# Kernel tuning notes

Hardware: AMD Instinct MI355X
Metric: run time of the kernel (lower is better)

Reference implementation:

```python
import jax, jax.numpy as jnp
import numpy as np

NOPE = 128          # qk_nope_head_dim
ROPE = 64           # qk_rope_head_dim
KV_LORA = 512       # kv_lora_rank
SCALE = (KV_LORA + ROPE) ** (-0.5)


def setup_inputs() -> dict:
    key = jax.random.key(0)
    k1, k2, k3, k4, k5 = jax.random.split(key, 5)
    T, H, K, S = 512, 128, 512, 8192
    q = jax.random.normal(k1, (T, H, NOPE + ROPE), dtype=jnp.float32)
    kv_cache = jax.random.normal(k2, (S, KV_LORA + ROPE), dtype=jnp.float32)
    topk_indices = jax.random.randint(k3, (T, K), 0, S, dtype=jnp.int32)
    k_b_proj_trans = jax.random.normal(k4, (H, KV_LORA, NOPE), dtype=jnp.float32) * 0.02
    v_b_proj = jax.random.normal(k5, (H, 128, KV_LORA), dtype=jnp.float32) * 0.02
    return {"q": q, "kv_cache": kv_cache, "topk_indices": topk_indices,
            "k_b_proj_trans": k_b_proj_trans, "v_b_proj": v_b_proj}


def reference(q, kv_cache, topk_indices, k_b_proj_trans, v_b_proj):
    # q: [T, H, 192]; kv_cache: [S, 576]; topk_indices: [T, K]
    q_nope, q_rope = q[..., :NOPE], q[..., NOPE:]
    # bmm_out(q_nope_t, k_b_proj_trans.transpose(1,2)): [T,H,128] x [H,512,128] -> [T,H,512]
    q_lat = jnp.einsum('thd,hkd->thk', q_nope, k_b_proj_trans)
    q_concat = jnp.concatenate([q_lat, q_rope], axis=-1)        # [T, H, 576]
    # sparse MLA: gather selected latent KV per token
    kv_sel = kv_cache[topk_indices]                              # [T, K, 576]
    scores = jnp.einsum('thc,tkc->thk', q_concat, kv_sel) * SCALE
    p = jax.nn.softmax(scores, axis=-1)                          # [T, H, K]
    attn_lat = jnp.einsum('thk,tkc->thc', p, kv_sel[..., :KV_LORA])  # [T, H, 512]
    # bmm_out(attn_lat_t, v_b_proj.transpose(1,2)): [T,H,512] x [H,512,128] -> [T,H,128]
    out = jnp.einsum('thc,hvc->thv', attn_lat, v_b_proj)
    return out
```

## Files before the change

kernel.cpp:

```cpp
#include <hip/hip_runtime.h>
#include <stdint.h>


#define SCALE 0.041666666666666664f

typedef __bf16 bf16x8 __attribute__((ext_vector_type(8)));
typedef float floatx4 __attribute__((ext_vector_type(4)));
typedef unsigned int uint32x2 __attribute__((ext_vector_type(2)));
typedef unsigned int uint32x4 __attribute__((ext_vector_type(4)));

static __device__ __forceinline__ unsigned short f2bf(float f) {
  unsigned int u = __builtin_bit_cast(unsigned int, f);
  u += 0x7FFF + ((u >> 16) & 1);
  return (unsigned short)(u >> 16);
}
static __device__ __forceinline__ float bf2f(unsigned short h) {
  unsigned int u = ((unsigned int)h) << 16;
  return __builtin_bit_cast(float, u);
}
static __device__ __forceinline__ unsigned int pack2(float lo, float hi) {
  return (unsigned int)f2bf(lo) | ((unsigned int)f2bf(hi) << 16);
}
static __device__ __forceinline__ void ldsdma16(const void* g, void* l) {
  __builtin_amdgcn_global_load_lds(
      (const __attribute__((address_space(1))) void*)g,
      (__attribute__((address_space(3))) void*)l, 16, 0, 0);
}
static __device__ __forceinline__ unsigned int lds_addr(const void* p) {
  return (unsigned int)(unsigned long long)(
      (__attribute__((address_space(3))) const void*)p);
}
#define TR64(dst, addr, OFF) \
  asm volatile("ds_read_b64_tr_b16 %0, %1 offset:" OFF : "=v"(dst) : "v"(addr))

static __device__ __forceinline__ void stage8_f32(const float* __restrict__ src,
                                                  unsigned short* dst) {
  const float4* s4 = reinterpret_cast<const float4*>(src);
  float4 v0 = s4[0], v1 = s4[1];
  uint4 o;
  o.x = pack2(v0.x, v0.y); o.y = pack2(v0.z, v0.w);
  o.z = pack2(v1.x, v1.y); o.w = pack2(v1.z, v1.w);
  *reinterpret_cast<uint4*>(dst) = o;
}

static __device__ __forceinline__ void mfma_4x4(const unsigned short* As,
                                                const unsigned short* Bs,
                                                int wm, int wn, int l15, int quad,
                                                floatx4 acc[4][4]) {
  bf16x8 af[4], bfr[4];
#pragma unroll
  for (int i = 0; i < 4; ++i)
    af[i] = *reinterpret_cast<const bf16x8*>(&As[(wm + i * 16 + l15) * 32 + quad * 8]);
#pragma unroll
  for (int j = 0; j < 4; ++j)
    bfr[j] = *reinterpret_cast<const bf16x8*>(&Bs[(wn + j * 16 + l15) * 32 + quad * 8]);
#pragma unroll
  for (int i = 0; i < 4; ++i)
#pragma unroll
    for (int j = 0; j < 4; ++j)
      acc[i][j] = __builtin_amdgcn_mfma_f32_16x16x32_bf16(af[i], bfr[j], acc[i][j], 0, 0, 0);
}

__global__ void prep(const float* __restrict__ kv, unsigned short* __restrict__ kvb,
                     const float* __restrict__ q, unsigned short* __restrict__ qc) {
  int b = blockIdx.x;
  if (b < 4608) {
    int i = b * 256 + threadIdx.x;
    float4 v = reinterpret_cast<const float4*>(kv)[i];
    ushort4 o;
    o.x = f2bf(v.x); o.y = f2bf(v.y); o.z = f2bf(v.z); o.w = f2bf(v.w);
    reinterpret_cast<ushort4*>(kvb)[i] = o;
  } else {
    int i = (b - 4608) * 256 + threadIdx.x;
    int r = i & 63;
    int th = i >> 6;
    qc[(size_t)th * 576 + 512 + r] = f2bf(q[(size_t)th * 192 + 128 + r] * SCALE);
  }
}

__global__ __launch_bounds__(256) void qlat_gemm(const float* __restrict__ q,
                                                 const float* __restrict__ kb,
                                                 unsigned short* __restrict__ qc) {
  const int h = blockIdx.x;
  const int tm = (blockIdx.y & 3) * 128;
  const int tn = (blockIdx.y >> 2) * 128;
  __shared__ __align__(16) unsigned short As[128 * 32];
  __shared__ __align__(16) unsigned short Bs[128 * 32];
  const int tid = threadIdx.x;
  const int lane = tid & 63, wave = tid >> 6;
  const int wm = (wave & 1) * 64, wn = (wave >> 1) * 64;
  const int l15 = lane & 15, quad = lane >> 4;
  const int r0 = tid >> 2, cg = tid & 3;
  const float* a0 = q + ((size_t)(tm + r0) * 128 + h) * 192 + cg * 8;
  const float* a1 = q + ((size_t)(tm + r0 + 64) * 128 + h) * 192 + cg * 8;
  const float* b0 = kb + ((size_t)h * 512 + tn + r0) * 128 + cg * 8;
  const float* b1 = b0 + (size_t)64 * 128;
  floatx4 acc[4][4] = {};
  for (int ks = 0; ks < 4; ++ks) {
    stage8_f32(a0 + ks * 32, &As[tid * 8]);
    stage8_f32(a1 + ks * 32, &As[2048 + tid * 8]);
    stage8_f32(b0 + ks * 32, &Bs[tid * 8]);
    stage8_f32(b1 + ks * 32, &Bs[2048 + tid * 8]);
    __syncthreads();
    mfma_4x4(As, Bs, wm, wn, l15, quad, acc);
    __syncthreads();
  }
#pragma unroll
  for (int i = 0; i < 4; ++i) {
    const int row = wm + i * 16 + quad * 4;
#pragma unroll
    for (int j = 0; j < 4; ++j) {
      const int col = wn + j * 16 + l15;
#pragma unroll
      for (int r = 0; r < 4; ++r) {
        const int t = tm + row + r;
        qc[((size_t)t * 128 + h) * 576 + tn + col] = f2bf(acc[i][j][r] * SCALE);
      }
    }
  }
}

__global__ __launch_bounds__(256) void scores_gemm(const unsigned short* __restrict__ qc,
                                                   const unsigned short* __restrict__ kvb,
                                                   const int* __restrict__ topk,
                                                   unsigned short* __restrict__ P) {
  const int t = blockIdx.x;
  const int tn = blockIdx.y * 128;
  __shared__ __align__(16) unsigned short As[2][128 * 32];
  __shared__ __align__(16) unsigned short Bs[2][128 * 32];
  const int tid = threadIdx.x;
  const int lane = tid & 63, wave = tid >> 6;
  const int wm = (wave & 1) * 64, wn = (wave >> 1) * 64;
  const int l15 = lane & 15, quad = lane >> 4;
  const int r0 = tid >> 2, cg = tid & 3;
  const unsigned short* a0 = qc + ((size_t)t * 128 + r0) * 576 + cg * 8;
  const unsigned short* a1 = a0 + (size_t)64 * 576;
  const int idx0 = topk[t * 512 + tn + r0];
  const int idx1 = topk[t * 512 + tn + r0 + 64];
  const unsigned short* b0 = kvb + (size_t)idx0 * 576 + cg * 8;
  const unsigned short* b1 = kvb + (size_t)idx1 * 576 + cg * 8;
  floatx4 acc[4][4] = {};
  ldsdma16(a0, &As[0][tid * 8]);
  ldsdma16(a1, &As[0][2048 + tid * 8]);
  ldsdma16(b0, &Bs[0][tid * 8]);
  ldsdma16(b1, &Bs[0][2048 + tid * 8]);
  __syncthreads();
  int cur = 0;
  for (int ks = 0; ks < 18; ++ks) {
    if (ks < 17) {
      ldsdma16(a0 + (ks + 1) * 32, &As[cur ^ 1][tid * 8]);
      ldsdma16(a1 + (ks + 1) * 32, &As[cur ^ 1][2048 + tid * 8]);
      ldsdma16(b0 + (ks + 1) * 32, &Bs[cur ^ 1][tid * 8]);
      ldsdma16(b1 + (ks + 1) * 32, &Bs[cur ^ 1][2048 + tid * 8]);
    }
    mfma_4x4(As[cur], Bs[cur], wm, wn, l15, quad, acc);
    __syncthreads();
    cur ^= 1;
  }
#pragma unroll
  for (int i = 0; i < 4; ++i) {
    const int row = wm + i * 16 + quad * 4;
#pragma unroll
    for (int j = 0; j < 4; ++j) {
      const int col = tn + wn + j * 16 + l15;
#pragma unroll
      for (int r = 0; r < 4; ++r)
        P[((size_t)t * 128 + row + r) * 512 + col] = f2bf(acc[i][j][r]);
    }
  }
}

__global__ __launch_bounds__(256) void softmax_rows(const unsigned short* __restrict__ Pin,
                                                    unsigned short* __restrict__ P2) {
  const int row = blockIdx.x * 4 + (threadIdx.x >> 6);
  const int t = row >> 7, h = row & 127;
  const int lane = threadIdx.x & 63;
  const unsigned short* rp = Pin + (size_t)row * 512 + lane * 8;
  uint4 raw = *reinterpret_cast<const uint4*>(rp);
  unsigned int w[4] = {raw.x, raw.y, raw.z, raw.w};
  float f[8];
  float mx = -1e30f;
#pragma unroll
  for (int i = 0; i < 8; ++i) {
    f[i] = bf2f((unsigned short)((w[i >> 1] >> ((i & 1) * 16)) & 0xFFFF));
    mx = fmaxf(mx, f[i]);
  }
#pragma unroll
  for (int off = 32; off; off >>= 1) mx = fmaxf(mx, __shfl_xor(mx, off, 64));
  float s = 0.f;
#pragma unroll
  for (int i = 0; i < 8; ++i) { f[i] = __expf(f[i] - mx); s += f[i]; }
#pragma unroll
  for (int off = 32; off; off >>= 1) s += __shfl_xor(s, off, 64);
  const float inv = 1.0f / s;
  uint4 o;
  o.x = pack2(f[0] * inv, f[1] * inv);
  o.y = pack2(f[2] * inv, f[3] * inv);
  o.z = pack2(f[4] * inv, f[5] * inv);
  o.w = pack2(f[6] * inv, f[7] * inv);
  unsigned short* wp =
      P2 + (((size_t)t * 16 + (lane >> 2)) * 128 + h) * 32 + (lane & 3) * 8;
  *reinterpret_cast<uint4*>(wp) = o;
}

__global__ __launch_bounds__(256) void attn_gemm(const unsigned short* __restrict__ P2,
                                                 const unsigned short* __restrict__ kvb,
                                                 const int* __restrict__ topk,
                                                 unsigned short* __restrict__ alat) {
  const int t = blockIdx.x;
  const int tn = blockIdx.y * 128;
  __shared__ __align__(16) unsigned short St[2][32 * 128];
  const int tid = threadIdx.x;
  const int lane = tid & 63, wave = tid >> 6;
  const int wm = (wave & 1) * 64, wn = (wave >> 1) * 64;
  const int l15 = lane & 15, quad = lane >> 4;
  const int keyA = wave * 4 + ((tid >> 1) & 3);
  const int cA = ((tid >> 3) & 7) * 16 + (tid & 1) * 8;
  const int* tkrow = topk + t * 512;
  const unsigned short* a_base =
      P2 + ((size_t)t * 16 * 128 + wm + l15) * 32 + quad * 8;
  const unsigned int tra0 = lds_addr(&St[0][0]) + quad * 2048 + wn * 8 + l15 * 8;
  floatx4 acc[4][4] = {};
  bf16x8 a_cur[4], a_nxt[4];
  int i0p, i1p;
  {
    const int i0 = tkrow[keyA];
    const int i1 = tkrow[16 + keyA];
    ldsdma16(kvb + (size_t)i0 * 576 + tn + cA, &St[0][tid * 8]);
    ldsdma16(kvb + (size_t)i1 * 576 + tn + cA, &St[0][2048 + tid * 8]);
    i0p = tkrow[32 + keyA];
    i1p = tkrow[48 + keyA];
#pragma unroll
    for (int i = 0; i < 4; ++i)
      a_cur[i] = *reinterpret_cast<const bf16x8*>(a_base + (size_t)i * 16 * 32);
  }
  __syncthreads();
  int cur = 0;
  for (int ks = 0; ks < 16; ++ks) {
    const unsigned int tra = tra0 + cur * 8192;
    uint32x2 r00, r01, r10, r11, r20, r21, r30, r31;
    TR64(r00, tra, "0");   TR64(r01, tra, "1024");
    TR64(r10, tra, "128"); TR64(r11, tra, "1152");
    TR64(r20, tra, "256"); TR64(r21, tra, "1280");
    TR64(r30, tra, "384"); TR64(r31, tra, "1408");
    if (ks < 15) {
      ldsdma16(kvb + (size_t)i0p * 576 + tn + cA, &St[cur ^ 1][tid * 8]);
      ldsdma16(kvb + (size_t)i1p * 576 + tn + cA, &St[cur ^ 1][2048 + tid * 8]);
#pragma unroll
      for (int i = 0; i < 4; ++i)
        a_nxt[i] = *reinterpret_cast<const bf16x8*>(
            a_base + ((size_t)(ks + 1) * 128 + i * 16) * 32);
      if (ks < 14) {
        i0p = tkrow[(ks + 2) * 32 + keyA];
        i1p = tkrow[(ks + 2) * 32 + 16 + keyA];
      }
    }
    asm volatile("s_waitcnt lgkmcnt(0)");
    __builtin_amdgcn_sched_barrier(0);
    bf16x8 bfr[4];
    {
      uint32x4 w;
      w.x = r00.x; w.y = r00.y; w.z = r01.x; w.w = r01.y;
      bfr[0] = __builtin_bit_cast(bf16x8, w);
      w.x = r10.x; w.y = r10.y; w.z = r11.x; w.w = r11.y;
      bfr[1] = __builtin_bit_cast(bf16x8, w);
      w.x = r20.x; w.y = r20.y; w.z = r21.x; w.w = r21.y;
      bfr[2] = __builtin_bit_cast(bf16x8, w);
      w.x = r30.x; w.y = r30.y; w.z = r31.x; w.w = r31.y;
      bfr[3] = __builtin_bit_cast(bf16x8, w);
    }
#pragma unroll
    for (int i = 0; i < 4; ++i)
#pragma unroll
      for (int j = 0; j < 4; ++j)
        acc[i][j] =
            __builtin_amdgcn_mfma_f32_16x16x32_bf16(a_cur[i], bfr[j], acc[i][j], 0, 0, 0);
    __syncthreads();
#pragma unroll
    for (int i = 0; i < 4; ++i) a_cur[i] = a_nxt[i];
    cur ^= 1;
  }
#pragma unroll
  for (int i = 0; i < 4; ++i) {
    const int row = wm + i * 16 + quad * 4;
#pragma unroll
    for (int j = 0; j < 4; ++j) {
      const int col = tn + wn + j * 16 + l15;
#pragma unroll
      for (int r = 0; r < 4; ++r)
        alat[((size_t)(row + r) * 512 + t) * 512 + col] = f2bf(acc[i][j][r]);
    }
  }
}

__global__ __launch_bounds__(256) void out_gemm(const unsigned short* __restrict__ alat,
                                                const float* __restrict__ vb,
                                                float* __restrict__ out) {
  const int h = blockIdx.x;
  const int tm = blockIdx.y * 128;
  __shared__ __align__(16) unsigned short As[128 * 32];
  __shared__ __align__(16) unsigned short Bs[128 * 32];
  const int tid = threadIdx.x;
  const int lane = tid & 63, wave = tid >> 6;
  const int wm = (wave & 1) * 64, wn = (wave >> 1) * 64;
  const int l15 = lane & 15, quad = lane >> 4;
  const int r0 = tid >> 2, cg = tid & 3;
  const unsigned short* a0 = alat + ((size_t)h * 512 + tm + r0) * 512 + cg * 8;
  const unsigned short* a1 = a0 + (size_t)64 * 512;
  const float* b0 = vb + ((size_t)h * 128 + r0) * 512 + cg * 8;
  const float* b1 = b0 + (size_t)64 * 512;
  floatx4 acc[4][4] = {};
  for (int ks = 0; ks < 16; ++ks) {
    ldsdma16(a0 + ks * 32, &As[tid * 8]);
    ldsdma16(a1 + ks * 32, &As[2048 + tid * 8]);
    stage8_f32(b0 + ks * 32, &Bs[tid * 8]);
    stage8_f32(b1 + ks * 32, &Bs[2048 + tid * 8]);
    __syncthreads();
    mfma_4x4(As, Bs, wm, wn, l15, quad, acc);
    __syncthreads();
  }
#pragma unroll
  for (int i = 0; i < 4; ++i) {
    const int row = wm + i * 16 + quad * 4;
#pragma unroll
    for (int j = 0; j < 4; ++j) {
      const int col = wn + j * 16 + l15;
#pragma unroll
      for (int r = 0; r < 4; ++r) {
        const int t = tm + row + r;
        out[((size_t)t * 128 + h) * 128 + col] = acc[i][j][r];
      }
    }
  }
}

extern "C" void kernel_launch(void* const* d_in, const int* in_sizes, int n_in,
                              void* d_out, int out_size, void* d_ws, size_t ws_size,
                              hipStream_t stream) {
  const float* q = (const float*)d_in[0];
  const float* kv = (const float*)d_in[1];
  const int* topk = (const int*)d_in[2];
  const float* kb = (const float*)d_in[3];
  const float* vb = (const float*)d_in[4];
  float* out = (float*)d_out;

  char* ws = (char*)d_ws;
  unsigned short* kvb = (unsigned short*)ws;
  unsigned short* qc = (unsigned short*)(ws + 9437184);
  unsigned short* P = (unsigned short*)(ws + 9437184 + 75497472);
  unsigned short* P2 = qc;
  unsigned short* alat = P;

  prep<<<dim3(20992), dim3(256), 0, stream>>>(kv, kvb, q, qc);
  qlat_gemm<<<dim3(128, 16), dim3(256), 0, stream>>>(q, kb, qc);
  scores_gemm<<<dim3(512, 4), dim3(256), 0, stream>>>(qc, kvb, topk, P);
  softmax_rows<<<dim3(16384), dim3(256), 0, stream>>>(P, P2);
  attn_gemm<<<dim3(512, 4), dim3(256), 0, stream>>>(P2, kvb, topk, alat);
  out_gemm<<<dim3(128, 4), dim3(256), 0, stream>>>(alat, vb, out);
}
```

Before: 385.4 us.

## Triple-buffer LDS DMA pipelines in scores and attention GEMMs

```diff
diff --git a/kernel.cpp b/kernel.cpp
--- a/kernel.cpp
+++ b/kernel.cpp
@@ -126,8 +126,8 @@
                                                    unsigned short* __restrict__ P) {
   const int t = blockIdx.x;
   const int tn = blockIdx.y * 128;
-  __shared__ __align__(16) unsigned short As[2][128 * 32];
-  __shared__ __align__(16) unsigned short Bs[2][128 * 32];
+  __shared__ __align__(16) unsigned short As[3][128 * 32];
+  __shared__ __align__(16) unsigned short Bs[3][128 * 32];
   const int tid = threadIdx.x;
   const int lane = tid & 63, wave = tid >> 6;
   const int wm = (wave & 1) * 64, wn = (wave >> 1) * 64;
@@ -140,22 +140,31 @@
   const unsigned short* b0 = kvb + (size_t)idx0 * 576 + cg * 8;
   const unsigned short* b1 = kvb + (size_t)idx1 * 576 + cg * 8;
   floatx4 acc[4][4] = {};
-  ldsdma16(a0, &As[0][tid * 8]);
-  ldsdma16(a1, &As[0][2048 + tid * 8]);
-  ldsdma16(b0, &Bs[0][tid * 8]);
-  ldsdma16(b1, &Bs[0][2048 + tid * 8]);
-  __syncthreads();
-  int cur = 0;
+#pragma unroll
+  for (int p = 0; p < 2; ++p) {
+    ldsdma16(a0 + p * 32, &As[p][tid * 8]);
+    ldsdma16(a1 + p * 32, &As[p][2048 + tid * 8]);
+    ldsdma16(b0 + p * 32, &Bs[p][tid * 8]);
+    ldsdma16(b1 + p * 32, &Bs[p][2048 + tid * 8]);
+  }
+  int bi = 0, bn = 2;
   for (int ks = 0; ks < 18; ++ks) {
-    if (ks < 17) {
-      ldsdma16(a0 + (ks + 1) * 32, &As[cur ^ 1][tid * 8]);
-      ldsdma16(a1 + (ks + 1) * 32, &As[cur ^ 1][2048 + tid * 8]);
-      ldsdma16(b0 + (ks + 1) * 32, &Bs[cur ^ 1][tid * 8]);
-      ldsdma16(b1 + (ks + 1) * 32, &Bs[cur ^ 1][2048 + tid * 8]);
-    }
-    mfma_4x4(As[cur], Bs[cur], wm, wn, l15, quad, acc);
-    __syncthreads();
-    cur ^= 1;
+    if (ks < 16) {
+      ldsdma16(a0 + (ks + 2) * 32, &As[bn][tid * 8]);
+      ldsdma16(a1 + (ks + 2) * 32, &As[bn][2048 + tid * 8]);
+      ldsdma16(b0 + (ks + 2) * 32, &Bs[bn][tid * 8]);
+      ldsdma16(b1 + (ks + 2) * 32, &Bs[bn][2048 + tid * 8]);
+      asm volatile("s_waitcnt vmcnt(8)" ::: "memory");
+    } else if (ks == 16) {
+      asm volatile("s_waitcnt vmcnt(4)" ::: "memory");
+    } else {
+      asm volatile("s_waitcnt vmcnt(0)" ::: "memory");
+    }
+    __builtin_amdgcn_s_barrier();
+    mfma_4x4(As[bi], Bs[bi], wm, wn, l15, quad, acc);
+    __builtin_amdgcn_s_barrier();
+    bi = bi == 2 ? 0 : bi + 1;
+    bn = bn == 2 ? 0 : bn + 1;
   }
 #pragma unroll
   for (int i = 0; i < 4; ++i) {
@@ -209,7 +218,7 @@
                                                  unsigned short* __restrict__ alat) {
   const int t = blockIdx.x;
   const int tn = blockIdx.y * 128;
-  __shared__ __align__(16) unsigned short St[2][32 * 128];
+  __shared__ __align__(16) unsigned short St[3][32 * 128];
   const int tid = threadIdx.x;
   const int lane = tid & 63, wave = tid >> 6;
   const int wm = (wave & 1) * 64, wn = (wave >> 1) * 64;
@@ -224,36 +233,43 @@
   bf16x8 a_cur[4], a_nxt[4];
   int i0p, i1p;
   {
-    const int i0 = tkrow[keyA];
-    const int i1 = tkrow[16 + keyA];
-    ldsdma16(kvb + (size_t)i0 * 576 + tn + cA, &St[0][tid * 8]);
-    ldsdma16(kvb + (size_t)i1 * 576 + tn + cA, &St[0][2048 + tid * 8]);
-    i0p = tkrow[32 + keyA];
-    i1p = tkrow[48 + keyA];
+    const int i00 = tkrow[keyA], i10 = tkrow[16 + keyA];
+    ldsdma16(kvb + (size_t)i00 * 576 + tn + cA, &St[0][tid * 8]);
+    ldsdma16(kvb + (size_t)i10 * 576 + tn + cA, &St[0][2048 + tid * 8]);
+    i0p = tkrow[64 + keyA];
+    i1p = tkrow[80 + keyA];
 #pragma unroll
     for (int i = 0; i < 4; ++i)
       a_cur[i] = *reinterpret_cast<const bf16x8*>(a_base + (size_t)i * 16 * 32);
-  }
-  __syncthreads();
-  int cur = 0;
+    const int i01 = tkrow[32 + keyA], i11 = tkrow[48 + keyA];
+    ldsdma16(kvb + (size_t)i01 * 576 + tn + cA, &St[1][tid * 8]);
+    ldsdma16(kvb + (size_t)i11 * 576 + tn + cA, &St[1][2048 + tid * 8]);
+  }
+  int sti = 0, std2 = 2;
   for (int ks = 0; ks < 16; ++ks) {
-    const unsigned int tra = tra0 + cur * 8192;
+    if (ks < 15) asm volatile("s_waitcnt vmcnt(2)" ::: "memory");
+    else         asm volatile("s_waitcnt vmcnt(0)" ::: "memory");
+    __builtin_amdgcn_s_barrier();
+    const unsigned int tra = tra0 + sti * 8192;
     uint32x2 r00, r01, r10, r11, r20, r21, r30, r31;
     TR64(r00, tra, "0");   TR64(r01, tra, "1024");
     TR64(r10, tra, "128"); TR64(r11, tra, "1152");
     TR64(r20, tra, "256"); TR64(r21, tra, "1280");
     TR64(r30, tra, "384"); TR64(r31, tra, "1408");
     if (ks < 15) {
-      ldsdma16(kvb + (size_t)i0p * 576 + tn + cA, &St[cur ^ 1][tid * 8]);
-      ldsdma16(kvb + (size_t)i1p * 576 + tn + cA, &St[cur ^ 1][2048 + tid * 8]);
 #pragma unroll
       for (int i = 0; i < 4; ++i)
         a_nxt[i] = *reinterpret_cast<const bf16x8*>(
             a_base + ((size_t)(ks + 1) * 128 + i * 16) * 32);
-      if (ks < 14) {
-        i0p = tkrow[(ks + 2) * 32 + keyA];
-        i1p = tkrow[(ks + 2) * 32 + 16 + keyA];
+    }
+    if (ks < 14) {
+      const int d0 = i0p, d1 = i1p;
+      if (ks < 13) {
+        i0p = tkrow[(ks + 3) * 32 + keyA];
+        i1p = tkrow[(ks + 3) * 32 + 16 + keyA];
       }
+      ldsdma16(kvb + (size_t)d0 * 576 + tn + cA, &St[std2][tid * 8]);
+      ldsdma16(kvb + (size_t)d1 * 576 + tn + cA, &St[std2][2048 + tid * 8]);
     }
     asm volatile("s_waitcnt lgkmcnt(0)");
     __builtin_amdgcn_sched_barrier(0);
@@ -275,10 +291,10 @@
       for (int j = 0; j < 4; ++j)
         acc[i][j] =
             __builtin_amdgcn_mfma_f32_16x16x32_bf16(a_cur[i], bfr[j], acc[i][j], 0, 0, 0);
-    __syncthreads();
 #pragma unroll
     for (int i = 0; i < 4; ++i) a_cur[i] = a_nxt[i];
-    cur ^= 1;
+    sti = sti == 2 ? 0 : sti + 1;
+    std2 = std2 == 2 ? 0 : std2 + 1;
   }
 #pragma unroll
   for (int i = 0; i < 4; ++i) {
```

Result: no change. 386.7 us (+0.3%).
